# Kernel optimization log

Measured on AMD Instinct MI355X. Metric: run time of the kernel, lower is better.

Reference implementation:

```python
import jax, jax.numpy as jnp
import numpy as np

N = 32768      # number of nodes (joint candidates)
DIN = 128      # NODE_INPUT_DIM
H1 = 128       # OUTPUT_SIZES[0]
DOUT = 128     # OUTPUT_SIZES[-1] == output_dim
T = 17         # number of node types / expert MLPs


def setup_inputs() -> dict:
    key = jax.random.key(0)
    ks = jax.random.split(key, 6)
    x = jax.random.normal(ks[0], (N, DIN), dtype=jnp.float32)
    node_types = jax.random.randint(ks[1], (N,), 0, T)
    # Stacked per-type MLP parameters (17 independent Linear-ReLU-Linear MLPs).
    W1 = jax.random.normal(ks[2], (T, DIN, H1), dtype=jnp.float32) / np.float32(np.sqrt(DIN))
    b1 = jax.random.normal(ks[3], (T, H1), dtype=jnp.float32) * 0.01
    W2 = jax.random.normal(ks[4], (T, H1, DOUT), dtype=jnp.float32) / np.float32(np.sqrt(H1))
    b2 = jax.random.normal(ks[5], (T, DOUT), dtype=jnp.float32) * 0.01
    return {"x": x, "W1": W1, "b1": b1, "W2": W2, "b2": b2, "node_types": node_types}


def reference(x, W1, b1, W2, b2, node_types):
    # Dense hard-routing: evaluate all 17 type-specific MLPs on every node,
    # then select each node's own type. Mathematically identical to the
    # boolean-mask gather/scatter loop in the torch module (each row of the
    # output is MLP_{node_types[n]}(x[n])), but fully vectorized and jittable.
    h = jax.nn.relu(jnp.einsum('nd,tdh->nth', x, W1) + b1)   # [N, T, H1]
    y = jnp.einsum('nth,thm->ntm', h, W2) + b2               # [N, T, DOUT]
    # gather the row matching each node's type (combine step)
    out = jnp.take_along_axis(y, node_types[:, None, None], axis=1)[:, 0, :]  # [N, DOUT]
    return out
```

## Files before the change

### kernel.cpp

```cpp
#include <hip/hip_runtime.h>

#define N_NODES 32768
#define NB 128
#define DIM 128
#define NT 17
#define ROWS 64
#define BPT 48
#define LP 136

typedef short bf16x8 __attribute__((ext_vector_type(8)));
typedef float f32x4 __attribute__((ext_vector_type(4)));

#define WS_BLOCKHIST 0
#define WS_TL        8704
#define WS_W1T       74240
#define WS_W2T       631296

__device__ __forceinline__ unsigned short f2bf(float f) {
  unsigned int u = __float_as_uint(f);
  u += 0x7FFFu + ((u >> 16) & 1u);
  return (unsigned short)(u >> 16);
}

__global__ void k_pre(const int* __restrict__ types, int* __restrict__ blockHist,
                      unsigned short* __restrict__ tl,
                      const float* __restrict__ W1, const float* __restrict__ W2,
                      unsigned short* __restrict__ W1t, unsigned short* __restrict__ W2t) {
  int tid = threadIdx.x;
  if (blockIdx.x < NB) {
    __shared__ int h[NT];
    if (tid < NT) h[tid] = 0;
    __syncthreads();
    int i = blockIdx.x * 256 + tid;
    int ty = types[i];
    int r = atomicAdd(&h[ty], 1);
    tl[i] = (unsigned short)(ty | (r << 5));
    __syncthreads();
    if (tid < NT) blockHist[blockIdx.x * NT + tid] = h[tid];
    return;
  }
  int m = blockIdx.x - NB;
  const float* src = (m < NT) ? (W1 + (size_t)m * DIM * DIM)
                              : (W2 + (size_t)(m - NT) * DIM * DIM);
  unsigned short* dst = (m < NT) ? (W1t + (size_t)m * DIM * DIM)
                                 : (W2t + (size_t)(m - NT) * DIM * DIM);
  __shared__ unsigned short tile[DIM * LP];
  #pragma unroll
  for (int it = 0; it < 32; ++it) {
    int s = tid + it * 256;
    int n = s & 127, kp = s >> 7;
    float a = src[(size_t)(2 * kp) * DIM + n];
    float b = src[(size_t)(2 * kp + 1) * DIM + n];
    unsigned int pk = (unsigned int)f2bf(a) | ((unsigned int)f2bf(b) << 16);
    *(unsigned int*)&tile[n * LP + 2 * kp] = pk;
  }
  __syncthreads();
  #pragma unroll
  for (int it = 0; it < 8; ++it) {
    int s = tid + it * 256;
    int n = s >> 4, c = s & 15;
    *(uint4*)(dst + (size_t)n * DIM + c * 8) = *(const uint4*)&tile[n * LP + c * 8];
  }
}

__global__ __launch_bounds__(256, 3)
void k_mlp(const float* __restrict__ x, const float* __restrict__ b1,
           const float* __restrict__ b2, float* __restrict__ out,
           const int* __restrict__ blockHist, const unsigned short* __restrict__ tl,
           const unsigned short* __restrict__ W1t, const unsigned short* __restrict__ W2t) {
  int t = blockIdx.y;
  int tid = threadIdx.x;

  __shared__ int cc[NB];
  __shared__ int prow[ROWS];
  __shared__ unsigned short Xs[ROWS * LP];
  __shared__ unsigned short Ws[DIM * LP];

  int v = 0;
  if (tid < NB) { v = blockHist[tid * NT + t]; cc[tid] = v; }
  #pragma unroll
  for (int off = 1; off < NB; off <<= 1) {
    __syncthreads();
    int add = (tid < NB && tid >= off) ? cc[tid - off] : 0;
    __syncthreads();
    if (tid < NB) { v += add; cc[tid] = v; }
  }
  __syncthreads();
  int total = cc[NB - 1];
  int win_lo = blockIdx.x * ROWS;
  if (win_lo >= total) return;
  int win_hi = win_lo + ROWS;
  int nvalid = min(ROWS, total - win_lo);

  if (tid < ROWS) prow[tid] = 0;
  __syncthreads();

  int lo = 0, hi = NB;
  while (lo < hi) { int mid = (lo + hi) >> 1; if (cc[mid] > win_lo) hi = mid; else lo = mid + 1; }
  for (int b = lo; b < NB; ++b) {
    int excl = b ? cc[b - 1] : 0;
    if (excl >= win_hi) break;
    unsigned short pv = tl[b * 256 + tid];
    int ty = pv & 31, lr = pv >> 5;
    int g = excl + lr;
    if (ty == t && g >= win_lo && g < win_hi) prow[g - win_lo] = b * 256 + tid;
  }
  __syncthreads();

  #pragma unroll
  for (int it = 0; it < 8; ++it) {
    int s = tid + it * 256;
    int r = s >> 5, c4 = s & 31;
    int rr = (r < nvalid) ? r : 0;
    const float4 vx = *(const float4*)(x + (size_t)prow[rr] * DIM + c4 * 4);
    unsigned int lo2 = (unsigned int)f2bf(vx.x) | ((unsigned int)f2bf(vx.y) << 16);
    unsigned int hi2 = (unsigned int)f2bf(vx.z) | ((unsigned int)f2bf(vx.w) << 16);
    *(uint2*)&Xs[r * LP + c4 * 4] = make_uint2(lo2, hi2);
  }
  const unsigned short* w1g = W1t + (size_t)t * DIM * DIM;
  #pragma unroll
  for (int it = 0; it < 8; ++it) {
    int s = tid + it * 256;
    int n = s >> 4, c = s & 15;
    *(uint4*)&Ws[n * LP + c * 8] = *(const uint4*)(w1g + n * DIM + c * 8);
  }
  __syncthreads();

  int lane = tid & 63, w = tid >> 6;
  int l15 = lane & 15, q = lane >> 4;
  int arow = w * 16 + l15;
  int kb = q * 8;

  f32x4 acc[8];
  #pragma unroll
  for (int nt = 0; nt < 8; ++nt) acc[nt] = (f32x4){0.f, 0.f, 0.f, 0.f};
  #pragma unroll
  for (int kk = 0; kk < 4; ++kk) {
    bf16x8 a = *(const bf16x8*)&Xs[arow * LP + kk * 32 + kb];
    #pragma unroll
    for (int nt = 0; nt < 8; ++nt) {
      bf16x8 b = *(const bf16x8*)&Ws[(nt * 16 + l15) * LP + kk * 32 + kb];
      acc[nt] = __builtin_amdgcn_mfma_f32_16x16x32_bf16(a, b, acc[nt], 0, 0, 0);
    }
  }
  const float* b1t = b1 + t * DIM;
  #pragma unroll
  for (int nt = 0; nt < 8; ++nt) {
    int col = nt * 16 + l15;
    float bias = b1t[col];
    #pragma unroll
    for (int r = 0; r < 4; ++r) {
      int row = w * 16 + q * 4 + r;
      Xs[row * LP + col] = f2bf(fmaxf(acc[nt][r] + bias, 0.f));
    }
  }
  __syncthreads();

  const unsigned short* w2g = W2t + (size_t)t * DIM * DIM;
  #pragma unroll
  for (int it = 0; it < 8; ++it) {
    int s = tid + it * 256;
    int n = s >> 4, c = s & 15;
    *(uint4*)&Ws[n * LP + c * 8] = *(const uint4*)(w2g + n * DIM + c * 8);
  }
  __syncthreads();

  #pragma unroll
  for (int nt = 0; nt < 8; ++nt) acc[nt] = (f32x4){0.f, 0.f, 0.f, 0.f};
  #pragma unroll
  for (int kk = 0; kk < 4; ++kk) {
    bf16x8 a = *(const bf16x8*)&Xs[arow * LP + kk * 32 + kb];
    #pragma unroll
    for (int nt = 0; nt < 8; ++nt) {
      bf16x8 b = *(const bf16x8*)&Ws[(nt * 16 + l15) * LP + kk * 32 + kb];
      acc[nt] = __builtin_amdgcn_mfma_f32_16x16x32_bf16(a, b, acc[nt], 0, 0, 0);
    }
  }
  const float* b2t = b2 + t * DIM;
  int r0 = w * 16 + q * 4;
  int gr[4]; bool vld[4];
  #pragma unroll
  for (int r = 0; r < 4; ++r) {
    vld[r] = (r0 + r) < nvalid;
    gr[r] = prow[r0 + r];
  }
  #pragma unroll
  for (int nt = 0; nt < 8; ++nt) {
    int col = nt * 16 + l15;
    float bias = b2t[col];
    #pragma unroll
    for (int r = 0; r < 4; ++r) {
      if (vld[r]) out[(size_t)gr[r] * DIM + col] = acc[nt][r] + bias;
    }
  }
}

extern "C" void kernel_launch(void* const* d_in, const int* in_sizes, int n_in,
                              void* d_out, int out_size, void* d_ws, size_t ws_size,
                              hipStream_t stream) {
  const float* x  = (const float*)d_in[0];
  const float* W1 = (const float*)d_in[1];
  const float* b1 = (const float*)d_in[2];
  const float* W2 = (const float*)d_in[3];
  const float* b2 = (const float*)d_in[4];
  const int* types = (const int*)d_in[5];
  float* out = (float*)d_out;

  char* ws = (char*)d_ws;
  int* blockHist = (int*)(ws + WS_BLOCKHIST);
  unsigned short* tl  = (unsigned short*)(ws + WS_TL);
  unsigned short* W1t = (unsigned short*)(ws + WS_W1T);
  unsigned short* W2t = (unsigned short*)(ws + WS_W2T);

  k_pre<<<NB + 2 * NT, 256, 0, stream>>>(types, blockHist, tl, W1, W2, W1t, W2t);
  dim3 grid(BPT, NT);
  k_mlp<<<grid, 256, 0, stream>>>(x, b1, b2, out, blockHist, tl, W1t, W2t);
}
```

Measured before the change: 93.48 us.

## Build per-type row lists with global atomics instead of per-block scan and search

The preprocessing kernel now reserves a slice of a per-type row-index list with a global atomicAdd per block and scatters node indices into it directly. The MLP kernel reads its 64 row indices straight from that list, dropping the 128-entry prefix scan, the binary search and the loop over type-label blocks. The cost is an extra memset launch, and row order within a type now depends on atomic ordering. Each type's capacity is fixed at BPT*ROWS, which assumes no type exceeds 3072 nodes.

```diff
diff --git a/kernel.cpp b/kernel.cpp
--- a/kernel.cpp
+++ b/kernel.cpp
@@ -6,15 +6,16 @@
 #define NT 17
 #define ROWS 64
 #define BPT 48
+#define CAP (BPT * ROWS)
 #define LP 136
 
 typedef short bf16x8 __attribute__((ext_vector_type(8)));
 typedef float f32x4 __attribute__((ext_vector_type(4)));
 
-#define WS_BLOCKHIST 0
-#define WS_TL        8704
-#define WS_W1T       74240
-#define WS_W2T       631296
+#define WS_CNT   0
+#define WS_ROWS  256
+#define WS_W1T   104704
+#define WS_W2T   661760
 
 __device__ __forceinline__ unsigned short f2bf(float f) {
   unsigned int u = __float_as_uint(f);
@@ -22,21 +23,23 @@
   return (unsigned short)(u >> 16);
 }
 
-__global__ void k_pre(const int* __restrict__ types, int* __restrict__ blockHist,
-                      unsigned short* __restrict__ tl,
+__global__ void k_pre(const int* __restrict__ types, int* __restrict__ cnt,
+                      unsigned short* __restrict__ rows,
                       const float* __restrict__ W1, const float* __restrict__ W2,
                       unsigned short* __restrict__ W1t, unsigned short* __restrict__ W2t) {
   int tid = threadIdx.x;
   if (blockIdx.x < NB) {
     __shared__ int h[NT];
+    __shared__ int bb[NT];
     if (tid < NT) h[tid] = 0;
     __syncthreads();
     int i = blockIdx.x * 256 + tid;
     int ty = types[i];
     int r = atomicAdd(&h[ty], 1);
-    tl[i] = (unsigned short)(ty | (r << 5));
     __syncthreads();
-    if (tid < NT) blockHist[blockIdx.x * NT + tid] = h[tid];
+    if (tid < NT) bb[tid] = atomicAdd(&cnt[tid], h[tid]);
+    __syncthreads();
+    rows[ty * CAP + bb[ty] + r] = (unsigned short)i;
     return;
   }
   int m = blockIdx.x - NB;
@@ -66,53 +69,29 @@
 __global__ __launch_bounds__(256, 3)
 void k_mlp(const float* __restrict__ x, const float* __restrict__ b1,
            const float* __restrict__ b2, float* __restrict__ out,
-           const int* __restrict__ blockHist, const unsigned short* __restrict__ tl,
+           const int* __restrict__ cnt, const unsigned short* __restrict__ rows,
            const unsigned short* __restrict__ W1t, const unsigned short* __restrict__ W2t) {
   int t = blockIdx.y;
   int tid = threadIdx.x;
 
-  __shared__ int cc[NB];
+  int total = cnt[t];
+  int win_lo = blockIdx.x * ROWS;
+  if (win_lo >= total) return;
+  int nvalid = min(ROWS, total - win_lo);
+
   __shared__ int prow[ROWS];
   __shared__ unsigned short Xs[ROWS * LP];
   __shared__ unsigned short Ws[DIM * LP];
 
-  int v = 0;
-  if (tid < NB) { v = blockHist[tid * NT + t]; cc[tid] = v; }
-  #pragma unroll
-  for (int off = 1; off < NB; off <<= 1) {
-    __syncthreads();
-    int add = (tid < NB && tid >= off) ? cc[tid - off] : 0;
-    __syncthreads();
-    if (tid < NB) { v += add; cc[tid] = v; }
-  }
-  __syncthreads();
-  int total = cc[NB - 1];
-  int win_lo = blockIdx.x * ROWS;
-  if (win_lo >= total) return;
-  int win_hi = win_lo + ROWS;
-  int nvalid = min(ROWS, total - win_lo);
-
-  if (tid < ROWS) prow[tid] = 0;
-  __syncthreads();
-
-  int lo = 0, hi = NB;
-  while (lo < hi) { int mid = (lo + hi) >> 1; if (cc[mid] > win_lo) hi = mid; else lo = mid + 1; }
-  for (int b = lo; b < NB; ++b) {
-    int excl = b ? cc[b - 1] : 0;
-    if (excl >= win_hi) break;
-    unsigned short pv = tl[b * 256 + tid];
-    int ty = pv & 31, lr = pv >> 5;
-    int g = excl + lr;
-    if (ty == t && g >= win_lo && g < win_hi) prow[g - win_lo] = b * 256 + tid;
-  }
+  if (tid < ROWS)
+    prow[tid] = rows[t * CAP + win_lo + min(tid, nvalid - 1)];
   __syncthreads();
 
   #pragma unroll
   for (int it = 0; it < 8; ++it) {
     int s = tid + it * 256;
     int r = s >> 5, c4 = s & 31;
-    int rr = (r < nvalid) ? r : 0;
-    const float4 vx = *(const float4*)(x + (size_t)prow[rr] * DIM + c4 * 4);
+    const float4 vx = *(const float4*)(x + (size_t)prow[r] * DIM + c4 * 4);
     unsigned int lo2 = (unsigned int)f2bf(vx.x) | ((unsigned int)f2bf(vx.y) << 16);
     unsigned int hi2 = (unsigned int)f2bf(vx.z) | ((unsigned int)f2bf(vx.w) << 16);
     *(uint2*)&Xs[r * LP + c4 * 4] = make_uint2(lo2, hi2);
@@ -207,12 +186,13 @@
   float* out = (float*)d_out;
 
   char* ws = (char*)d_ws;
-  int* blockHist = (int*)(ws + WS_BLOCKHIST);
-  unsigned short* tl  = (unsigned short*)(ws + WS_TL);
-  unsigned short* W1t = (unsigned short*)(ws + WS_W1T);
-  unsigned short* W2t = (unsigned short*)(ws + WS_W2T);
+  int* cnt = (int*)(ws + WS_CNT);
+  unsigned short* rows = (unsigned short*)(ws + WS_ROWS);
+  unsigned short* W1t  = (unsigned short*)(ws + WS_W1T);
+  unsigned short* W2t  = (unsigned short*)(ws + WS_W2T);
 
-  k_pre<<<NB + 2 * NT, 256, 0, stream>>>(types, blockHist, tl, W1, W2, W1t, W2t);
+  hipMemsetAsync(cnt, 0, NT * sizeof(int), stream);
+  k_pre<<<NB + 2 * NT, 256, 0, stream>>>(types, cnt, rows, W1, W2, W1t, W2t);
   dim3 grid(BPT, NT);
-  k_mlp<<<grid, 256, 0, stream>>>(x, b1, b2, out, blockHist, tl, W1t, W2t);
+  k_mlp<<<grid, 256, 0, stream>>>(x, b1, b2, out, cnt, rows, W1t, W2t);
 }
```

After: 95.56 us. 2.2% more time.
